# Optimization experiments

Hardware: AMD Instinct MI355X
Metric: run time of the kernel (lower is better)

The kernel has to match this reference:

```python
import jax, jax.numpy as jnp
import numpy as np
from jax import lax

IMG_SELECT = np.linspace(0, 367, 112, dtype=int)  # static gather indices


def _make_wavelet_bank():
    """Real parts of the 112 Morlet wavelet filters, zero-padded (centered) to a
    common odd length K so a single grouped-as-multi-channel conv reproduces the
    per-filter SAME-padded Conv1d outputs exactly."""
    dt = 0.004
    w = 6.0
    coeff = np.sqrt(w * w + 2)
    scales = np.reciprocal(np.arange(40, 4, -36 / 112)) * (coeff + w) / (4.0 * np.pi)
    filts = []
    for scale in scales:
        M = 10 * scale / dt
        t = np.arange((-M + 1) / 2.0, (M + 1) / 2.0) * dt
        if len(t) % 2 == 0:
            t = t[:-1]
        norm = (dt / scale) ** 0.5
        xx = t / scale
        wav = np.exp(1j * w * xx) - np.exp(-0.5 * w ** 2)
        wav *= np.exp(-0.5 * xx ** 2) * np.pi ** (-0.25)
        # .type(torch.FloatTensor) on the complex cwt keeps only the real part,
        # so only the real filter channels contribute to the output.
        filts.append((norm * wav).real.astype(np.float32))
    K = max(len(f) for f in filts)
    if K % 2 == 0:
        K += 1
    W = np.zeros((len(filts), 1, K), np.float32)  # [112, 1, K]
    for i, f in enumerate(filts):
        p = (K - len(f)) // 2
        W[i, 0, p:p + len(f)] = f
    return W


def setup_inputs() -> dict:
    key = jax.random.key(0)
    ks = jax.random.split(key, 14)
    B = 2048
    x = jax.random.normal(ks[0], (B, 1, 368), dtype=jnp.float32)

    def rn(k, shape, scale=0.1):
        return jax.random.normal(k, shape, dtype=jnp.float32) * scale

    return {
        "x": x,
        "wavelet_w": jnp.asarray(_make_wavelet_bank()),
        "conv1_w": rn(ks[1], (6, 1, 3, 3)), "conv1_b": rn(ks[2], (6,)),
        "conv2_w": rn(ks[3], (12, 6, 3, 3)), "conv2_b": rn(ks[4], (12,)),
        "conv3_w": rn(ks[5], (12, 12, 3, 3)), "conv3_b": rn(ks[6], (12,)),
        "conv4_w": rn(ks[7], (12, 12, 3, 3)), "conv4_b": rn(ks[8], (12,)),
        "fc1_w": rn(ks[9], (48, 588)), "fc1_b": rn(ks[10], (48,)),
        "fc2_w": rn(ks[11], (4, 48)), "fc2_b": rn(ks[12], (4,)),
    }


def _conv2d(h, w, b):
    out = lax.conv_general_dilated(h, w, (1, 1), 'SAME',
                                   dimension_numbers=('NCHW', 'OIHW', 'NCHW'))
    return out + b[None, :, None, None]


def _maxpool2(h):
    return lax.reduce_window(h, -jnp.inf, lax.max, (1, 1, 2, 2), (1, 1, 2, 2), 'VALID')


def reference(x, wavelet_w, conv1_w, conv1_b, conv2_w, conv2_b, conv3_w, conv3_b,
              conv4_w, conv4_b, fc1_w, fc1_b, fc2_w, fc2_b):
    # Fused multi-scale wavelet filter bank: one conv, 112 output channels.
    K = wavelet_w.shape[-1]
    pad = (K - 1) // 2
    cwt = lax.conv_general_dilated(x, wavelet_w, (1,), [(pad, pad)],
                                   dimension_numbers=('NCH', 'OIH', 'NCH'))  # [B,112,368]
    img = cwt[:, :, IMG_SELECT][:, None]  # [B,1,112,112] (resize_ == reshape here)

    # Dense CNN stack (dropout is identity in eval mode).
    h = _maxpool2(jax.nn.relu(_conv2d(img, conv1_w, conv1_b)))  # [B,6,56,56]
    h = _maxpool2(jax.nn.relu(_conv2d(h, conv2_w, conv2_b)))    # [B,12,28,28]
    h = _maxpool2(jax.nn.relu(_conv2d(h, conv3_w, conv3_b)))    # [B,12,14,14]
    h = _maxpool2(jax.nn.relu(_conv2d(h, conv4_w, conv4_b)))    # [B,12,7,7]
    h = h.reshape(h.shape[0], -1)                               # [B,588]
    h = jax.nn.relu(h @ fc1_w.T + fc1_b)                        # [B,48]
    return jax.nn.softmax(h @ fc2_w.T + fc2_b, axis=-1)         # [B,4]
```

## Files before the change

kernel.cpp:

```cpp
#include <hip/hip_runtime.h>

#define NTH  512
#define XLEN 368
#define NF   112

typedef short bh8 __attribute__((ext_vector_type(8)));
typedef float fv4 __attribute__((ext_vector_type(4)));
typedef float f32x2 __attribute__((ext_vector_type(2)));

#define IMG_OFF 0
#define IMG_LD  114
#define X0H 12996
#define X1H 14020
#define H1_OFF 15044
#define TOT_E 35228

#define H2_OFF 0
#define H3_OFF 10800
#define H4_F 0
#define FC1_F 600
#define LG_F 652

#define KA_TOT 15044
#define KB1_TOT 26912
#define T_H3 14400
#define KB2_TOT 18496

__device__ __forceinline__ unsigned short bfbits(float v) {
  union { __bf16 b; unsigned short u; } c;
  c.b = (__bf16)v;
  return c.u;
}
__device__ __forceinline__ float f_lo(unsigned u) {
  return __uint_as_float(u << 16);
}
__device__ __forceinline__ float f_hi(unsigned u) {
  return __uint_as_float(u & 0xffff0000u);
}

__global__ void prep_A(const float* __restrict__ ww, int K, int nks,
                       bh8* __restrict__ Aarr) {
  int idx = blockIdx.x * 256 + threadIdx.x;
  int total = 7 * nks * 64;
  if (idx >= total) return;
  int lane = idx & 63;
  int fk = idx >> 6;
  int ks = fk % nks, ft = fk / nks;
  int frow = ft * 16 + (lane & 15);
  int k0 = ks * 32 + 8 * (lane >> 4);
  union { bh8 s; unsigned short h[8]; } o;
  #pragma unroll
  for (int e = 0; e < 8; ++e) {
    int k = k0 + e;
    float v = (k < K) ? ww[(size_t)frow * K + k] : 0.f;
    o.h[e] = bfbits(v);
  }
  Aarr[idx] = o.s;
}

__global__ void prep_bounds(const float* __restrict__ ww, int K, int nks,
                            int* __restrict__ bnd) {
  __shared__ int slo[256], shi[256];
  int ft = blockIdx.x, t = threadIdx.x;
  int lo = K, hi = -1;
  for (int m = t; m < 16 * K; m += 256) {
    int f = ft * 16 + m / K, k = m % K;
    if (ww[(size_t)f * K + k] != 0.f) { lo = min(lo, k); hi = max(hi, k); }
  }
  slo[t] = lo; shi[t] = hi;
  __syncthreads();
  for (int s = 128; s > 0; s >>= 1) {
    if (t < s) {
      slo[t] = min(slo[t], slo[t + s]);
      shi[t] = max(shi[t], shi[t + s]);
    }
    __syncthreads();
  }
  if (t == 0) {
    int l = slo[0], h = shi[0];
    if (h < 0) { bnd[2 * ft] = 0; bnd[2 * ft + 1] = 0; }
    else {
      bnd[2 * ft] = l >> 5;
      bnd[2 * ft + 1] = min((h >> 5) + 1, nks);
    }
  }
}

__global__ void prep_W1(const float* __restrict__ f1w,
                        bh8* __restrict__ w1f) {
  int idx = blockIdx.x * 256 + threadIdx.x;
  if (idx >= 3648) return;
  int lane = idx & 63;
  int fk = idx >> 6;
  int ks = fk % 19, ft = fk / 19;
  int oc = ft * 16 + (lane & 15);
  int k0 = ks * 32 + (lane >> 4) * 8;
  union { bh8 s; unsigned short h[8]; } o;
  #pragma unroll
  for (int e = 0; e < 8; ++e) {
    int k = k0 + e;
    o.h[e] = (k < 588) ? bfbits(f1w[(size_t)oc * 588 + k])
                       : (unsigned short)0;
  }
  w1f[idx] = o.s;
}

__global__ void prep_Wc(const float* __restrict__ c2w,
                        const float* __restrict__ c3w,
                        const float* __restrict__ c4w,
                        bh8* __restrict__ wcf) {
  int idx = blockIdx.x * 256 + threadIdx.x;
  if (idx >= 832) return;
  int lane = idx & 63;
  int fr = idx >> 6;
  int oc = lane & 15;
  int koff = (lane >> 4) * 8;
  union { bh8 s; unsigned short h[8]; } o;
  if (fr < 3) {
    #pragma unroll
    for (int e = 0; e < 8; ++e) {
      int k = fr * 32 + koff + e;
      int tap = k >> 3, ic = k & 7;
      float v = (oc < 12 && tap < 9 && ic < 6)
                    ? c2w[(oc * 6 + ic) * 9 + tap] : 0.f;
      o.h[e] = bfbits(v);
    }
  } else {
    int m = (fr < 8) ? (fr - 3) : (fr - 8);
    const float* w = (fr < 8) ? c3w : c4w;
    #pragma unroll
    for (int e = 0; e < 8; ++e) {
      int k = m * 32 + koff + e;
      int tap = k >> 4, ic = k & 15;
      float v = (oc < 12 && tap < 9 && ic < 12)
                    ? w[(oc * 12 + ic) * 9 + tap] : 0.f;
      o.h[e] = bfbits(v);
    }
  }
  wcf[idx] = o.s;
}

__device__ __forceinline__ void conv4acc(const float (&p)[4][4],
                                         const float (&w9)[9],
                                         float (&acc)[4]) {
  #pragma unroll
  for (int dy = 0; dy < 2; ++dy)
    #pragma unroll
    for (int dx = 0; dx < 2; ++dx) {
      float a = 0.f;
      #pragma unroll
      for (int dr = 0; dr < 3; ++dr)
        #pragma unroll
        for (int dc = 0; dc < 3; ++dc)
          a = fmaf(p[dy + dr][dx + dc], w9[dr * 3 + dc], a);
      acc[dy * 2 + dx] += a;
    }
}

__device__ __forceinline__ void load_patch(const unsigned short* su, int baseEl,
                                           int ldEl, float (&p)[4][4]) {
  #pragma unroll
  for (int i = 0; i < 4; ++i) {
    unsigned a = *(const unsigned*)(su + baseEl + i * ldEl);
    unsigned b = *(const unsigned*)(su + baseEl + i * ldEl + 2);
    p[i][0] = f_lo(a); p[i][1] = f_hi(a);
    p[i][2] = f_lo(b); p[i][3] = f_hi(b);
  }
}

template <bool PRE>
__device__ __forceinline__ void cwt_phase(unsigned short* su, int tid,
                                          const float* __restrict__ ww,
                                          const bh8* __restrict__ Aarr,
                                          const int* __restrict__ bnd,
                                          int K, int nks) {
  const int wid = __builtin_amdgcn_readfirstlane(tid >> 6);
  const int lane = tid & 63;
  const int koff = (lane >> 4) * 8;
  #pragma unroll 1
  for (int tile = wid; tile < 49; tile += NTH / 64) {
    const int ft = tile / 7, jt = tile - ft * 7;
    int klo = 0, khi = nks;
    if (PRE) { klo = bnd[2 * ft]; khi = bnd[2 * ft + 1]; }
    const int jcol = jt * 16 + (lane & 15);
    const int selj = (jcol == NF - 1)
        ? (XLEN - 1)
        : (int)((double)jcol * ((double)(XLEN - 1) / (double)(NF - 1)));
    fv4 acc = {0.f, 0.f, 0.f, 0.f};
    for (int ks = klo; ks < khi; ++ks) {
      const int kbase = selj + (ks << 5) + koff;
      const int par = kbase & 1;
      const int e0 = kbase - par;
      const unsigned* ph = (const unsigned*)(su + (par ? X1H : X0H) + e0);
      union { bh8 v; unsigned u[4]; } bh_;
      #pragma unroll
      for (int j = 0; j < 4; ++j) bh_.u[j] = ph[j];
      bh8 ah;
      if (PRE) {
        ah = Aarr[((size_t)ft * nks + ks) * 64 + lane];
      } else {
        const int frow = ft * 16 + (lane & 15);
        union { bh8 s; unsigned short h[8]; } ha;
        #pragma unroll
        for (int e = 0; e < 8; ++e) {
          int k = (ks << 5) + koff + e;
          float v = (k < K) ? ww[(size_t)frow * K + k] : 0.f;
          ha.h[e] = bfbits(v);
        }
        ah = ha.s;
      }
      acc = __builtin_amdgcn_mfma_f32_16x16x32_bf16(ah, bh_.v, acc, 0, 0, 0);
    }
    const int col = jt * 16 + (lane & 15) + 1;
    const int fbase = ft * 16 + (lane >> 4) * 4 + 1;
    #pragma unroll
    for (int r = 0; r < 4; ++r)
      su[IMG_OFF + (fbase + r) * IMG_LD + col] = bfbits(acc[r]);
  }
}

__global__ __launch_bounds__(NTH, 4) void k_cwt_conv1(
    const float* __restrict__ x, const bh8* __restrict__ Aarr,
    const int* __restrict__ bnd, int K, int nks,
    const float* __restrict__ c1w, const float* __restrict__ c1b,
    unsigned* __restrict__ h1g) {
  extern __shared__ unsigned short su[];
  const int b = blockIdx.x;
  const int tid = threadIdx.x;
  const int pad = (K - 1) >> 1;

  for (int m = tid; m < 452; m += NTH) {
    int r, c;
    if (m < 114) { r = 0; c = m; }
    else if (m < 228) { r = 113; c = m - 114; }
    else if (m < 340) { r = m - 228 + 1; c = 0; }
    else { r = m - 340 + 1; c = 113; }
    su[IMG_OFF + r * IMG_LD + c] = 0;
  }
  for (int i = tid; i < 1024; i += NTH) {
    float f0 = 0.f, f1 = 0.f;
    int xi = i - pad;
    if (xi >= 0 && xi < XLEN) f0 = x[(size_t)b * XLEN + xi];
    if (xi + 1 >= 0 && xi + 1 < XLEN) f1 = x[(size_t)b * XLEN + xi + 1];
    su[X0H + i] = bfbits(f0);
    su[X1H + i] = bfbits(f1);
  }
  __syncthreads();

  cwt_phase<true>(su, tid, nullptr, Aarr, bnd, K, nks);
  __syncthreads();

  unsigned* h1s = h1g + (size_t)b * 9408;
  float wAll[54], bAll[6];
  #pragma unroll
  for (int t = 0; t < 54; ++t) wAll[t] = c1w[t];
  #pragma unroll
  for (int o = 0; o < 6; ++o) bAll[o] = c1b[o];
  for (int it = tid; it < 3136; it += NTH) {
    int pr = it / 56, pc = it - pr * 56;
    float p[4][4];
    load_patch(su, IMG_OFF + (pr * 2) * IMG_LD + pc * 2, IMG_LD, p);
    f32x2 pq[4][3];
    #pragma unroll
    for (int r = 0; r < 4; ++r)
      #pragma unroll
      for (int c = 0; c < 3; ++c) pq[r][c] = f32x2{p[r][c], p[r][c + 1]};
    union { unsigned w[3]; unsigned short h[6]; } ou;
    #pragma unroll
    for (int oc = 0; oc < 6; ++oc) {
      f32x2 a0 = {bAll[oc], bAll[oc]};
      f32x2 a1 = a0;
      #pragma unroll
      for (int dr = 0; dr < 3; ++dr)
        #pragma unroll
        for (int dc = 0; dc < 3; ++dc) {
          float w = wAll[oc * 9 + dr * 3 + dc];
          f32x2 wv = {w, w};
          a0 = __builtin_elementwise_fma(pq[dr][dc], wv, a0);
          a1 = __builtin_elementwise_fma(pq[dr + 1][dc], wv, a1);
        }
      float m = fmaxf(fmaxf(a0.x, a0.y), fmaxf(a1.x, a1.y));
      ou.h[oc] = bfbits(fmaxf(m, 0.f));
    }
    h1s[it] = ou.w[0];
    h1s[3136 + it] = ou.w[1];
    h1s[6272 + it] = ou.w[2];
  }
}

__global__ __launch_bounds__(NTH, 4) void k_conv2(
    const unsigned* __restrict__ h1g, const bh8* __restrict__ wcf,
    const float* __restrict__ c2b, unsigned* __restrict__ h2g) {
  extern __shared__ unsigned short su[];
  unsigned* su32 = (unsigned*)su;
  const int b = blockIdx.x;
  const int tid = threadIdx.x;
  const int lane = tid & 63, wid = tid >> 6;
  const int oc_a = lane & 15;
  const int row0 = (lane >> 4) * 4;

  for (int m = tid; m < 228; m += NTH) {
    int r, c;
    if (m < 58) { r = 0; c = m; }
    else if (m < 116) { r = 57; c = m - 58; }
    else if (m < 172) { r = m - 116 + 1; c = 0; }
    else { r = m - 172 + 1; c = 57; }
    ((uint4*)su)[r * 58 + c] = uint4{0, 0, 0, 0};
  }
  {
    const unsigned* g = h1g + (size_t)b * 9408;
    for (int i2 = tid; i2 < 9408; i2 += NTH) {
      int plane = i2 / 3136, pt = i2 - plane * 3136;
      int pr = pt / 56, pc = pt - pr * 56;
      su32[((pr + 1) * 58 + (pc + 1)) * 4 + plane] = g[i2];
    }
    for (int pt = tid; pt < 3136; pt += NTH) {
      int pr = pt / 56, pc = pt - pr * 56;
      su32[((pr + 1) * 58 + (pc + 1)) * 4 + 3] = 0;
    }
  }
  bh8 afr[3];
  #pragma unroll
  for (int m = 0; m < 3; ++m) afr[m] = wcf[m * 64 + lane];
  float biasv[4];
  #pragma unroll
  for (int r = 0; r < 4; ++r)
    biasv[r] = (row0 + r < 12) ? c2b[row0 + r] : 0.f;
  __syncthreads();

  unsigned* h2s = h2g + (size_t)b * 4704;
  for (int t = wid; t < 196; t += NTH / 64) {
    int n = t * 16 + oc_a;
    int p = n >> 2, q = n & 3;
    int pr = p / 28, pc = p - pr * 28;
    int r = pr * 2 + (q >> 1), c = pc * 2 + (q & 1);
    int base = (r * 58 + c) * 8;
    fv4 acc = {biasv[0], biasv[1], biasv[2], biasv[3]};
    #pragma unroll
    for (int m = 0; m < 3; ++m) {
      int tap = m * 4 + (lane >> 4);
      if (tap > 8) tap = 8;
      int dr = tap / 3, dc = tap - dr * 3;
      bh8 bv = *(const bh8*)(su + base + (dr * 58 + dc) * 8);
      acc = __builtin_amdgcn_mfma_f32_16x16x32_bf16(afr[m], bv, acc, 0, 0, 0);
    }
    union { uint2 v; unsigned short h[4]; } ou;
    #pragma unroll
    for (int r4 = 0; r4 < 4; ++r4) {
      float v = acc[r4];
      v = fmaxf(v, __shfl_xor(v, 1));
      v = fmaxf(v, __shfl_xor(v, 2));
      ou.h[r4] = bfbits(fmaxf(v, 0.f));
    }
    if ((lane & 3) == 0 && row0 < 12) {
      int w = row0 >> 1;
      h2s[w * 784 + p] = ou.v.x;
      h2s[(w + 1) * 784 + p] = ou.v.y;
    }
  }
}

__global__ __launch_bounds__(NTH, 4) void k_tail(
    const unsigned* __restrict__ h2g, const bh8* __restrict__ wcf,
    const float* __restrict__ c3b, const float* __restrict__ c4b,
    unsigned short* __restrict__ h4g) {
  extern __shared__ unsigned short su[];
  unsigned* su32 = (unsigned*)su;
  const int b = blockIdx.x;
  const int tid = threadIdx.x;
  const int lane = tid & 63, wid = tid >> 6;
  const int oc_a = lane & 15;
  const int koff = (lane >> 4) * 8;
  const int row0 = (lane >> 4) * 4;
  const int icoff = koff & 15;
  const int taphalf = koff >> 4;

  for (int m = tid; m < 116; m += NTH) {
    int r, c;
    if (m < 30) { r = 0; c = m; }
    else if (m < 60) { r = 29; c = m - 30; }
    else if (m < 88) { r = m - 60 + 1; c = 0; }
    else { r = m - 88 + 1; c = 29; }
    ((uint4*)su)[(r * 30 + c) * 2] = uint4{0, 0, 0, 0};
    ((uint4*)su)[(r * 30 + c) * 2 + 1] = uint4{0, 0, 0, 0};
  }
  for (int m = tid; m < 60; m += NTH) {
    int r, c;
    if (m < 16) { r = 0; c = m; }
    else if (m < 32) { r = 15; c = m - 16; }
    else if (m < 46) { r = m - 32 + 1; c = 0; }
    else { r = m - 46 + 1; c = 15; }
    ((uint4*)(su + T_H3))[(r * 16 + c) * 2] = uint4{0, 0, 0, 0};
    ((uint4*)(su + T_H3))[(r * 16 + c) * 2 + 1] = uint4{0, 0, 0, 0};
  }
  {
    const unsigned* g = h2g + (size_t)b * 4704;
    for (int i2 = tid; i2 < 4704; i2 += NTH) {
      int plane = i2 / 784, pt = i2 - plane * 784;
      int pr = pt / 28, pc = pt - pr * 28;
      su32[((pr + 1) * 30 + (pc + 1)) * 8 + plane] = g[i2];
    }
    for (int m = tid; m < 1568; m += NTH) {
      int pt = m >> 1, w = 6 + (m & 1);
      int pr = pt / 28, pc = pt - pr * 28;
      su32[((pr + 1) * 30 + (pc + 1)) * 8 + w] = 0;
    }
  }
  bh8 a3[5], a4[5];
  #pragma unroll
  for (int m = 0; m < 5; ++m) a3[m] = wcf[(3 + m) * 64 + lane];
  #pragma unroll
  for (int m = 0; m < 5; ++m) a4[m] = wcf[(8 + m) * 64 + lane];
  float bias3[4], bias4[4];
  #pragma unroll
  for (int r = 0; r < 4; ++r) {
    bias3[r] = (row0 + r < 12) ? c3b[row0 + r] : 0.f;
    bias4[r] = (row0 + r < 12) ? c4b[row0 + r] : 0.f;
  }
  __syncthreads();

  for (int t = wid; t < 49; t += NTH / 64) {
    int n = t * 16 + oc_a;
    int p = n >> 2, q = n & 3;
    int pr = p / 14, pc = p - pr * 14;
    int r = pr * 2 + (q >> 1), c = pc * 2 + (q & 1);
    int base = (r * 30 + c) * 16 + icoff;
    fv4 acc = {bias3[0], bias3[1], bias3[2], bias3[3]};
    #pragma unroll
    for (int m = 0; m < 5; ++m) {
      int tap = m * 2 + taphalf;
      if (tap > 8) tap = 8;
      int dr = tap / 3, dc = tap - dr * 3;
      bh8 bv = *(const bh8*)(su + base + (dr * 30 + dc) * 16);
      acc = __builtin_amdgcn_mfma_f32_16x16x32_bf16(a3[m], bv, acc, 0, 0, 0);
    }
    union { uint2 v; unsigned short h[4]; } ou;
    #pragma unroll
    for (int r4 = 0; r4 < 4; ++r4) {
      float v = acc[r4];
      v = fmaxf(v, __shfl_xor(v, 1));
      v = fmaxf(v, __shfl_xor(v, 2));
      ou.h[r4] = bfbits(fmaxf(v, 0.f));
    }
    if ((lane & 3) == 0)
      *(uint2*)(su + T_H3 + ((pr + 1) * 16 + (pc + 1)) * 16 + row0) = ou.v;
  }
  __syncthreads();

  unsigned short* h4s = h4g + (size_t)b * 608;
  for (int t = wid; t < 13; t += NTH / 64) {
    int n = t * 16 + oc_a;
    int p = n >> 2, q = n & 3;
    int pp = (p < 49) ? p : 0;
    int pr = pp / 7, pc = pp - pr * 7;
    int r = pr * 2 + (q >> 1), c = pc * 2 + (q & 1);
    int base = T_H3 + (r * 16 + c) * 16 + icoff;
    fv4 acc = {bias4[0], bias4[1], bias4[2], bias4[3]};
    #pragma unroll
    for (int m = 0; m < 5; ++m) {
      int tap = m * 2 + taphalf;
      if (tap > 8) tap = 8;
      int dr = tap / 3, dc = tap - dr * 3;
      bh8 bv = *(const bh8*)(su + base + (dr * 16 + dc) * 16);
      acc = __builtin_amdgcn_mfma_f32_16x16x32_bf16(a4[m], bv, acc, 0, 0, 0);
    }
    #pragma unroll
    for (int r4 = 0; r4 < 4; ++r4) {
      float v = acc[r4];
      v = fmaxf(v, __shfl_xor(v, 1));
      v = fmaxf(v, __shfl_xor(v, 2));
      v = fmaxf(v, 0.f);
      int oc = row0 + r4;
      if ((lane & 3) == 0 && p < 49 && oc < 12)
        h4s[oc * 49 + pr * 7 + pc] = bfbits(v);
    }
  }
}

__global__ __launch_bounds__(64) void k_fc(
    const unsigned short* __restrict__ h4g, const bh8* __restrict__ w1f,
    const float* __restrict__ f1b, const float* __restrict__ f2w,
    const float* __restrict__ f2b, int nsamp, float* __restrict__ out) {
  __shared__ float fcs[16][49];
  const int lane = threadIdx.x;
  const int sbase = blockIdx.x * 16;
  const int scol = lane & 15;
  const int koff = (lane >> 4) * 8;
  const int row0 = (lane >> 4) * 4;
  int srow = sbase + scol;
  if (srow >= nsamp) srow = nsamp - 1;
  const unsigned short* hrow = h4g + (size_t)srow * 608 + koff;

  fv4 acc[3];
  #pragma unroll
  for (int ft = 0; ft < 3; ++ft) acc[ft] = fv4{0.f, 0.f, 0.f, 0.f};
  for (int ks = 0; ks < 19; ++ks) {
    bh8 bv = *(const bh8*)(hrow + ks * 32);
    #pragma unroll
    for (int ft = 0; ft < 3; ++ft) {
      bh8 av = w1f[(ft * 19 + ks) * 64 + lane];
      acc[ft] = __builtin_amdgcn_mfma_f32_16x16x32_bf16(av, bv, acc[ft],
                                                        0, 0, 0);
    }
  }
  #pragma unroll
  for (int ft = 0; ft < 3; ++ft)
    #pragma unroll
    for (int r = 0; r < 4; ++r) {
      int oc = ft * 16 + row0 + r;
      fcs[scol][oc] = fmaxf(acc[ft][r] + f1b[oc], 0.f);
    }
  __syncthreads();
  if (lane < 16 && sbase + lane < nsamp) {
    float l[4];
    #pragma unroll
    for (int o = 0; o < 4; ++o) {
      float s = f2b[o];
      for (int i = 0; i < 48; ++i) s += fcs[lane][i] * f2w[o * 48 + i];
      l[o] = s;
    }
    float m = fmaxf(fmaxf(l[0], l[1]), fmaxf(l[2], l[3]));
    float e0 = expf(l[0] - m), e1 = expf(l[1] - m);
    float e2 = expf(l[2] - m), e3 = expf(l[3] - m);
    float ss = e0 + e1 + e2 + e3;
    float* o4 = out + (size_t)(sbase + lane) * 4;
    o4[0] = e0 / ss; o4[1] = e1 / ss; o4[2] = e2 / ss; o4[3] = e3 / ss;
  }
}

template <int NKS, int KREAL, int NOC, int OMODE>
__device__ __forceinline__ void conv_mfma(
    unsigned short* su, float* sfl, unsigned short* gout, int tid,
    int inOff, int inLD, int inCh,
    int outOff, int outLD, int outCh, int plW,
    int NT, int NPOOL,
    const float* __restrict__ wgt, const float* __restrict__ bias) {
  const int lane = tid & 63;
  const int wid = tid >> 6;
  const int oc_a = lane & 15;
  const int koff = (lane >> 4) * 8;
  const int row0 = (lane >> 4) * 4;

  bh8 afr[NKS];
  unsigned opk[NKS][4];
  #pragma unroll
  for (int ks = 0; ks < NKS; ++ks) {
    union { bh8 s; unsigned short h[8]; } au;
    #pragma unroll
    for (int e = 0; e < 8; ++e) {
      int k = ks * 32 + koff + e;
      au.h[e] = (oc_a < NOC && k < KREAL)
                    ? bfbits(wgt[oc_a * KREAL + k]) : (unsigned short)0;
    }
    afr[ks] = au.s;
    #pragma unroll
    for (int e2 = 0; e2 < 4; ++e2) {
      unsigned o01[2];
      #pragma unroll
      for (int h = 0; h < 2; ++h) {
        int k = ks * 32 + koff + 2 * e2 + h;
        int kc = (k < KREAL) ? k : 0;
        int ic = kc / 9, rem = kc - ic * 9;
        o01[h] = (unsigned)(ic * inCh + (rem / 3) * inLD +
                            (rem - (rem / 3) * 3));
      }
      opk[ks][e2] = o01[0] | (o01[1] << 16);
    }
  }
  float biasv[4];
  #pragma unroll
  for (int r = 0; r < 4; ++r)
    biasv[r] = (row0 + r < NOC) ? bias[row0 + r] : 0.f;

  for (int t = wid; t < NT; t += NTH / 64) {
    int n = t * 16 + oc_a;
    int p = n >> 2, q = n & 3;
    int pp = (p < NPOOL) ? p : 0;
    int pr = pp / plW, pc = pp - pr * plW;
    int r = pr * 2 + (q >> 1), c = pc * 2 + (q & 1);
    int base = inOff + r * inLD + c;
    fv4 acc = {biasv[0], biasv[1], biasv[2], biasv[3]};
    #pragma unroll
    for (int ks = 0; ks < NKS; ++ks) {
      union { bh8 v; unsigned short h[8]; } bu;
      #pragma unroll
      for (int e2 = 0; e2 < 4; ++e2) {
        unsigned pk = opk[ks][e2];
        bu.h[2 * e2] = su[base + (pk & 0xffffu)];
        bu.h[2 * e2 + 1] = su[base + (pk >> 16)];
      }
      acc = __builtin_amdgcn_mfma_f32_16x16x32_bf16(afr[ks], bu.v, acc, 0, 0, 0);
    }
    #pragma unroll
    for (int r4 = 0; r4 < 4; ++r4) {
      float v = acc[r4];
      v = fmaxf(v, __shfl_xor(v, 1));
      v = fmaxf(v, __shfl_xor(v, 2));
      v = fmaxf(v, 0.f);
      int oc = row0 + r4;
      if ((lane & 3) == 0 && oc < NOC && p < NPOOL) {
        if (OMODE == 1)
          sfl[outOff + oc * (plW * plW) + pr * plW + pc] = v;
        else if (OMODE == 2)
          gout[oc * NPOOL + pr * plW + pc] = bfbits(v);
        else
          su[outOff + oc * outCh + (pr + 1) * outLD + (pc + 1)] = bfbits(v);
      }
    }
  }
}

template <bool PRE>
__global__ __launch_bounds__(NTH, 4) void fused_convnet(
    const float* __restrict__ x, const float* __restrict__ ww,
    const bh8* __restrict__ Aarr, const int* __restrict__ bnd,
    int K, int nks,
    const float* __restrict__ c1w, const float* __restrict__ c1b,
    const float* __restrict__ c2w, const float* __restrict__ c2b,
    const float* __restrict__ c3w, const float* __restrict__ c3b,
    const float* __restrict__ c4w, const float* __restrict__ c4b,
    const float* __restrict__ f1w, const float* __restrict__ f1b,
    const float* __restrict__ f2w, const float* __restrict__ f2b,
    float* __restrict__ out) {
  extern __shared__ unsigned short su[];
  float* sfl = (float*)su;
  const int b = blockIdx.x;
  const int tid = threadIdx.x;
  const int pad = (K - 1) >> 1;

  for (int m = tid; m < 452; m += NTH) {
    int r, c;
    if (m < 114) { r = 0; c = m; }
    else if (m < 228) { r = 113; c = m - 114; }
    else if (m < 340) { r = m - 228 + 1; c = 0; }
    else { r = m - 340 + 1; c = 113; }
    su[IMG_OFF + r * IMG_LD + c] = 0;
  }
  for (int m = tid; m < 1368; m += NTH) {
    int ch = m / 228, w = m - ch * 228, r, c;
    if (w < 58) { r = 0; c = w; }
    else if (w < 116) { r = 57; c = w - 58; }
    else if (w < 172) { r = w - 116 + 1; c = 0; }
    else { r = w - 172 + 1; c = 57; }
    su[H1_OFF + ch * 3364 + r * 58 + c] = 0;
  }
  for (int i = tid; i < 1024; i += NTH) {
    float f0 = 0.f, f1 = 0.f;
    int xi = i - pad;
    if (xi >= 0 && xi < XLEN) f0 = x[(size_t)b * XLEN + xi];
    if (xi + 1 >= 0 && xi + 1 < XLEN) f1 = x[(size_t)b * XLEN + xi + 1];
    su[X0H + i] = bfbits(f0);
    su[X1H + i] = bfbits(f1);
  }
  __syncthreads();

  cwt_phase<PRE>(su, tid, ww, Aarr, bnd, K, nks);
  __syncthreads();

  for (int it = tid; it < 3136; it += NTH) {
    int pr = it / 56, pc = it - pr * 56;
    float p[4][4];
    load_patch(su, IMG_OFF + (pr * 2) * IMG_LD + pc * 2, IMG_LD, p);
    #pragma unroll
    for (int oc = 0; oc < 6; ++oc) {
      float w9[9];
      #pragma unroll
      for (int t = 0; t < 9; ++t) w9[t] = c1w[oc * 9 + t];
      float acc[4] = {c1b[oc], c1b[oc], c1b[oc], c1b[oc]};
      conv4acc(p, w9, acc);
      float m = fmaxf(fmaxf(acc[0], acc[1]), fmaxf(acc[2], acc[3]));
      su[H1_OFF + oc * 3364 + (pr + 1) * 58 + (pc + 1)] = bfbits(fmaxf(m, 0.f));
    }
  }
  __syncthreads();

  for (int m = tid; m < 1392; m += NTH) {
    int ch = m / 116, w = m - ch * 116, r, c;
    if (w < 30) { r = 0; c = w; }
    else if (w < 60) { r = 29; c = w - 30; }
    else if (w < 88) { r = w - 60 + 1; c = 0; }
    else { r = w - 88 + 1; c = 29; }
    su[H2_OFF + ch * 900 + r * 30 + c] = 0;
  }
  for (int m = tid; m < 720; m += NTH) {
    int ch = m / 60, w = m - ch * 60, r, c;
    if (w < 16) { r = 0; c = w; }
    else if (w < 32) { r = 15; c = w - 16; }
    else if (w < 46) { r = w - 32 + 1; c = 0; }
    else { r = w - 46 + 1; c = 15; }
    su[H3_OFF + ch * 256 + r * 16 + c] = 0;
  }
  __syncthreads();

  conv_mfma<2, 54, 12, 0>(su, sfl, nullptr, tid, H1_OFF, 58, 3364,
                          H2_OFF, 30, 900, 28, 196, 784, c2w, c2b);
  __syncthreads();

  conv_mfma<4, 108, 12, 0>(su, sfl, nullptr, tid, H2_OFF, 30, 900,
                           H3_OFF, 16, 256, 14, 49, 196, c3w, c3b);
  __syncthreads();

  conv_mfma<4, 108, 12, 1>(su, sfl, nullptr, tid, H3_OFF, 16, 256,
                           H4_F, 0, 0, 7, 13, 49, c4w, c4b);
  __syncthreads();

  {
    int wv = tid >> 6, ln = tid & 63;
    for (int o = wv; o < 48; o += NTH / 64) {
      float s = 0.f;
      for (int i = ln; i < 588; i += 64)
        s += sfl[H4_F + i] * f1w[(size_t)o * 588 + i];
      #pragma unroll
      for (int off = 32; off > 0; off >>= 1) s += __shfl_down(s, off);
      if (ln == 0) sfl[FC1_F + o] = fmaxf(s + f1b[o], 0.f);
    }
  }
  __syncthreads();
  if (tid < 4) {
    float s = f2b[tid];
    for (int i = 0; i < 48; ++i) s += sfl[FC1_F + i] * f2w[tid * 48 + i];
    sfl[LG_F + tid] = s;
  }
  __syncthreads();
  if (tid < 4) {
    float l0 = sfl[LG_F + 0], l1 = sfl[LG_F + 1];
    float l2 = sfl[LG_F + 2], l3 = sfl[LG_F + 3];
    float m = fmaxf(fmaxf(l0, l1), fmaxf(l2, l3));
    float e0 = expf(l0 - m), e1 = expf(l1 - m);
    float e2 = expf(l2 - m), e3 = expf(l3 - m);
    float ssum = e0 + e1 + e2 + e3;
    out[(size_t)b * 4 + tid] = expf(sfl[LG_F + tid] - m) / ssum;
  }
}

extern "C" void kernel_launch(void* const* d_in, const int* in_sizes, int n_in,
                              void* d_out, int out_size, void* d_ws,
                              size_t ws_size, hipStream_t stream) {
  const float* x   = (const float*)d_in[0];
  const float* ww  = (const float*)d_in[1];
  const float* c1w = (const float*)d_in[2];
  const float* c1b = (const float*)d_in[3];
  const float* c2w = (const float*)d_in[4];
  const float* c2b = (const float*)d_in[5];
  const float* c3w = (const float*)d_in[6];
  const float* c3b = (const float*)d_in[7];
  const float* c4w = (const float*)d_in[8];
  const float* c4b = (const float*)d_in[9];
  const float* f1w = (const float*)d_in[10];
  const float* f1b = (const float*)d_in[11];
  const float* f2w = (const float*)d_in[12];
  const float* f2b = (const float*)d_in[13];
  float* out = (float*)d_out;

  const int B = in_sizes[0] / XLEN;
  const int K = in_sizes[1] / NF;
  const int nks = (K + 31) / 32;

  const int items = 7 * nks * 64;
  const size_t aoff = (size_t)items * sizeof(bh8);
  const size_t abytes = aoff + 64;
  const size_t w1off = abytes;
  const size_t w1bytes = (size_t)3648 * sizeof(bh8);
  const size_t wcoff = w1off + w1bytes;
  const size_t wcbytes = (size_t)832 * sizeof(bh8);
  const size_t h1off = wcoff + wcbytes;
  const size_t h1bytes = (size_t)B * 18816 * 2;
  const size_t h2off = h1off + h1bytes;
  const size_t h2bytes = (size_t)B * 9408 * 2;
  const size_t h4off = h2off + h2bytes;
  const size_t h4bytes = (size_t)B * 608 * 2;
  const size_t need3 = h4off + h4bytes;

  bh8* Aarr = (bh8*)d_ws;
  int* bnd = (int*)((char*)d_ws + aoff);
  bh8* w1f = (bh8*)((char*)d_ws + w1off);
  bh8* wcf = (bh8*)((char*)d_ws + wcoff);
  unsigned* h1g = (unsigned*)((char*)d_ws + h1off);
  unsigned* h2g = (unsigned*)((char*)d_ws + h2off);
  unsigned short* h4g = (unsigned short*)((char*)d_ws + h4off);

  if (ws_size >= need3) {
    hipLaunchKernelGGL(prep_A, dim3((items + 255) / 256), dim3(256), 0, stream,
                       ww, K, nks, Aarr);
    hipLaunchKernelGGL(prep_bounds, dim3(7), dim3(256), 0, stream,
                       ww, K, nks, bnd);
    hipLaunchKernelGGL(prep_W1, dim3(15), dim3(256), 0, stream, f1w, w1f);
    hipLaunchKernelGGL(prep_Wc, dim3(4), dim3(256), 0, stream,
                       c2w, c3w, c4w, wcf);
    hipFuncSetAttribute((const void*)k_cwt_conv1,
                        hipFuncAttributeMaxDynamicSharedMemorySize,
                        KA_TOT * 2);
    hipFuncSetAttribute((const void*)k_conv2,
                        hipFuncAttributeMaxDynamicSharedMemorySize,
                        KB1_TOT * 2);
    hipFuncSetAttribute((const void*)k_tail,
                        hipFuncAttributeMaxDynamicSharedMemorySize,
                        KB2_TOT * 2);
    hipLaunchKernelGGL(k_cwt_conv1, dim3(B), dim3(NTH), KA_TOT * 2, stream,
                       x, Aarr, bnd, K, nks, c1w, c1b, h1g);
    hipLaunchKernelGGL(k_conv2, dim3(B), dim3(NTH), KB1_TOT * 2, stream,
                       h1g, wcf, c2b, h2g);
    hipLaunchKernelGGL(k_tail, dim3(B), dim3(NTH), KB2_TOT * 2, stream,
                       h2g, wcf, c3b, c4b, h4g);
    hipLaunchKernelGGL(k_fc, dim3((B + 15) / 16), dim3(64), 0, stream,
                       h4g, w1f, f1b, f2w, f2b, B, out);
  } else if (ws_size >= abytes) {
    hipLaunchKernelGGL(prep_A, dim3((items + 255) / 256), dim3(256), 0, stream,
                       ww, K, nks, Aarr);
    hipLaunchKernelGGL(prep_bounds, dim3(7), dim3(256), 0, stream,
                       ww, K, nks, bnd);
    hipFuncSetAttribute((const void*)fused_convnet<true>,
                        hipFuncAttributeMaxDynamicSharedMemorySize,
                        TOT_E * 2);
    hipLaunchKernelGGL(fused_convnet<true>, dim3(B), dim3(NTH), TOT_E * 2,
                       stream, x, ww, Aarr, bnd, K, nks, c1w, c1b, c2w, c2b,
                       c3w, c3b, c4w, c4b, f1w, f1b, f2w, f2b, out);
  } else {
    hipFuncSetAttribute((const void*)fused_convnet<false>,
                        hipFuncAttributeMaxDynamicSharedMemorySize,
                        TOT_E * 2);
    hipLaunchKernelGGL(fused_convnet<false>, dim3(B), dim3(NTH), TOT_E * 2,
                       stream, x, ww, Aarr, bnd, K, nks, c1w, c1b, c2w, c2b,
                       c3w, c3b, c4w, c4b, f1w, f1b, f2w, f2b, out);
  }
}
```

Baseline: 192.7 us.

## Fuse conv2 into the CWT/conv1 kernel using two half-image passes

Merges the separate conv2 kernel into the front kernel, so conv2 runs right after conv1 in the same block. Because the shared-memory budget stays at the smaller front-kernel size, conv2 processes the 56x56 conv1 output in two 28-row halves with halo rows, re-reading h1 from global memory (now likely L2-resident since the same block just wrote it). The conv1 weights are read straight from global instead of being preloaded into 54 registers, which lowers register pressure. The intent is to drop a kernel launch and improve locality of the h1 round trip, at the cost of an extra barrier per half and a longer kernel.

```diff
diff --git a/kernel.cpp b/kernel.cpp
--- a/kernel.cpp
+++ b/kernel.cpp
@@ -22,7 +22,6 @@
 #define LG_F 652
 
 #define KA_TOT 15044
-#define KB1_TOT 26912
 #define T_H3 14400
 #define KB2_TOT 18496
 
@@ -219,14 +218,17 @@
   }
 }
 
-__global__ __launch_bounds__(NTH, 4) void k_cwt_conv1(
+__global__ __launch_bounds__(NTH, 4) void k_front(
     const float* __restrict__ x, const bh8* __restrict__ Aarr,
     const int* __restrict__ bnd, int K, int nks,
     const float* __restrict__ c1w, const float* __restrict__ c1b,
-    unsigned* __restrict__ h1g) {
+    const bh8* __restrict__ wcf, const float* __restrict__ c2b,
+    unsigned* __restrict__ h1g, unsigned* __restrict__ h2g) {
   extern __shared__ unsigned short su[];
+  unsigned* su32 = (unsigned*)su;
   const int b = blockIdx.x;
   const int tid = threadIdx.x;
+  const int lane = tid & 63, wid = tid >> 6;
   const int pad = (K - 1) >> 1;
 
   for (int m = tid; m < 452; m += NTH) {
@@ -251,11 +253,6 @@
   __syncthreads();
 
   unsigned* h1s = h1g + (size_t)b * 9408;
-  float wAll[54], bAll[6];
-  #pragma unroll
-  for (int t = 0; t < 54; ++t) wAll[t] = c1w[t];
-  #pragma unroll
-  for (int o = 0; o < 6; ++o) bAll[o] = c1b[o];
   for (int it = tid; it < 3136; it += NTH) {
     int pr = it / 56, pc = it - pr * 56;
     float p[4][4];
@@ -268,13 +265,13 @@
     union { unsigned w[3]; unsigned short h[6]; } ou;
     #pragma unroll
     for (int oc = 0; oc < 6; ++oc) {
-      f32x2 a0 = {bAll[oc], bAll[oc]};
+      f32x2 a0 = {c1b[oc], c1b[oc]};
       f32x2 a1 = a0;
       #pragma unroll
       for (int dr = 0; dr < 3; ++dr)
         #pragma unroll
         for (int dc = 0; dc < 3; ++dc) {
-          float w = wAll[oc * 9 + dr * 3 + dc];
+          float w = c1w[oc * 9 + dr * 3 + dc];
           f32x2 wv = {w, w};
           a0 = __builtin_elementwise_fma(pq[dr][dc], wv, a0);
           a1 = __builtin_elementwise_fma(pq[dr + 1][dc], wv, a1);
@@ -286,39 +283,9 @@
     h1s[3136 + it] = ou.w[1];
     h1s[6272 + it] = ou.w[2];
   }
-}
-
-__global__ __launch_bounds__(NTH, 4) void k_conv2(
-    const unsigned* __restrict__ h1g, const bh8* __restrict__ wcf,
-    const float* __restrict__ c2b, unsigned* __restrict__ h2g) {
-  extern __shared__ unsigned short su[];
-  unsigned* su32 = (unsigned*)su;
-  const int b = blockIdx.x;
-  const int tid = threadIdx.x;
-  const int lane = tid & 63, wid = tid >> 6;
+
   const int oc_a = lane & 15;
   const int row0 = (lane >> 4) * 4;
-
-  for (int m = tid; m < 228; m += NTH) {
-    int r, c;
-    if (m < 58) { r = 0; c = m; }
-    else if (m < 116) { r = 57; c = m - 58; }
-    else if (m < 172) { r = m - 116 + 1; c = 0; }
-    else { r = m - 172 + 1; c = 57; }
-    ((uint4*)su)[r * 58 + c] = uint4{0, 0, 0, 0};
-  }
-  {
-    const unsigned* g = h1g + (size_t)b * 9408;
-    for (int i2 = tid; i2 < 9408; i2 += NTH) {
-      int plane = i2 / 3136, pt = i2 - plane * 3136;
-      int pr = pt / 56, pc = pt - pr * 56;
-      su32[((pr + 1) * 58 + (pc + 1)) * 4 + plane] = g[i2];
-    }
-    for (int pt = tid; pt < 3136; pt += NTH) {
-      int pr = pt / 56, pc = pt - pr * 56;
-      su32[((pr + 1) * 58 + (pc + 1)) * 4 + 3] = 0;
-    }
-  }
   bh8 afr[3];
   #pragma unroll
   for (int m = 0; m < 3; ++m) afr[m] = wcf[m * 64 + lane];
@@ -326,36 +293,51 @@
   #pragma unroll
   for (int r = 0; r < 4; ++r)
     biasv[r] = (row0 + r < 12) ? c2b[row0 + r] : 0.f;
-  __syncthreads();
-
   unsigned* h2s = h2g + (size_t)b * 4704;
-  for (int t = wid; t < 196; t += NTH / 64) {
-    int n = t * 16 + oc_a;
-    int p = n >> 2, q = n & 3;
-    int pr = p / 28, pc = p - pr * 28;
-    int r = pr * 2 + (q >> 1), c = pc * 2 + (q & 1);
-    int base = (r * 58 + c) * 8;
-    fv4 acc = {biasv[0], biasv[1], biasv[2], biasv[3]};
-    #pragma unroll
-    for (int m = 0; m < 3; ++m) {
-      int tap = m * 4 + (lane >> 4);
-      if (tap > 8) tap = 8;
-      int dr = tap / 3, dc = tap - dr * 3;
-      bh8 bv = *(const bh8*)(su + base + (dr * 58 + dc) * 8);
-      acc = __builtin_amdgcn_mfma_f32_16x16x32_bf16(afr[m], bv, acc, 0, 0, 0);
-    }
-    union { uint2 v; unsigned short h[4]; } ou;
-    #pragma unroll
-    for (int r4 = 0; r4 < 4; ++r4) {
-      float v = acc[r4];
-      v = fmaxf(v, __shfl_xor(v, 1));
-      v = fmaxf(v, __shfl_xor(v, 2));
-      ou.h[r4] = bfbits(fmaxf(v, 0.f));
-    }
-    if ((lane & 3) == 0 && row0 < 12) {
-      int w = row0 >> 1;
-      h2s[w * 784 + p] = ou.v.x;
-      h2s[(w + 1) * 784 + p] = ou.v.y;
+
+  #pragma unroll 1
+  for (int half = 0; half < 2; ++half) {
+    const int rbase = half * 28 - 1;
+    __syncthreads();
+    for (int i = tid; i < 5220; i += NTH) {
+      int plane = i / 1740, rem = i - plane * 1740;
+      int lr = rem / 58, cc = rem - lr * 58;
+      int hr = rbase + lr, hc = cc - 1;
+      unsigned v = (hr >= 0 && hr < 56 && hc >= 0 && hc < 56)
+                       ? h1s[plane * 3136 + hr * 56 + hc] : 0u;
+      su32[(lr * 58 + cc) * 4 + plane] = v;
+    }
+    for (int i = tid; i < 1740; i += NTH) su32[i * 4 + 3] = 0;
+    __syncthreads();
+    for (int t = wid; t < 98; t += NTH / 64) {
+      int n = t * 16 + oc_a;
+      int p = n >> 2, q = n & 3;
+      int lpr = p / 28, lpc = p - lpr * 28;
+      int r = lpr * 2 + (q >> 1), c = lpc * 2 + (q & 1);
+      int base = (r * 58 + c) * 8;
+      fv4 acc = {biasv[0], biasv[1], biasv[2], biasv[3]};
+      #pragma unroll
+      for (int m = 0; m < 3; ++m) {
+        int tap = m * 4 + (lane >> 4);
+        if (tap > 8) tap = 8;
+        int dr = tap / 3, dc = tap - dr * 3;
+        bh8 bv = *(const bh8*)(su + base + (dr * 58 + dc) * 8);
+        acc = __builtin_amdgcn_mfma_f32_16x16x32_bf16(afr[m], bv, acc, 0, 0, 0);
+      }
+      union { uint2 v; unsigned short h[4]; } ou;
+      #pragma unroll
+      for (int r4 = 0; r4 < 4; ++r4) {
+        float v = acc[r4];
+        v = fmaxf(v, __shfl_xor(v, 1));
+        v = fmaxf(v, __shfl_xor(v, 2));
+        ou.h[r4] = bfbits(fmaxf(v, 0.f));
+      }
+      if ((lane & 3) == 0 && row0 < 12) {
+        int gp = (lpr + half * 14) * 28 + lpc;
+        int w = row0 >> 1;
+        h2s[w * 784 + gp] = ou.v.x;
+        h2s[(w + 1) * 784 + gp] = ou.v.y;
+      }
     }
   }
 }
@@ -787,19 +769,14 @@
     hipLaunchKernelGGL(prep_W1, dim3(15), dim3(256), 0, stream, f1w, w1f);
     hipLaunchKernelGGL(prep_Wc, dim3(4), dim3(256), 0, stream,
                        c2w, c3w, c4w, wcf);
-    hipFuncSetAttribute((const void*)k_cwt_conv1,
+    hipFuncSetAttribute((const void*)k_front,
                         hipFuncAttributeMaxDynamicSharedMemorySize,
                         KA_TOT * 2);
-    hipFuncSetAttribute((const void*)k_conv2,
-                        hipFuncAttributeMaxDynamicSharedMemorySize,
-                        KB1_TOT * 2);
     hipFuncSetAttribute((const void*)k_tail,
                         hipFuncAttributeMaxDynamicSharedMemorySize,
                         KB2_TOT * 2);
-    hipLaunchKernelGGL(k_cwt_conv1, dim3(B), dim3(NTH), KA_TOT * 2, stream,
-                       x, Aarr, bnd, K, nks, c1w, c1b, h1g);
-    hipLaunchKernelGGL(k_conv2, dim3(B), dim3(NTH), KB1_TOT * 2, stream,
-                       h1g, wcf, c2b, h2g);
+    hipLaunchKernelGGL(k_front, dim3(B), dim3(NTH), KA_TOT * 2, stream,
+                       x, Aarr, bnd, K, nks, c1w, c1b, wcf, c2b, h1g, h2g);
     hipLaunchKernelGGL(k_tail, dim3(B), dim3(NTH), KB2_TOT * 2, stream,
                        h2g, wcf, c3b, c4b, h4g);
     hipLaunchKernelGGL(k_fc, dim3((B + 15) / 16), dim3(64), 0, stream,
```

Result: slower. 198.9 us (+3.2%).
